# Optimization experiments

Measured on AMD Instinct MI355X. Metric: run time of the kernel, lower is better.

## Reference

```python
import jax, jax.numpy as jnp
import numpy as np

B, N, K = 8, 4096, 64          # graphs, nodes per graph, clusters
E_PER = 65536                   # edges per graph (avg degree 16)
EPS = 1e-15


def gcn_conv(x, W, b, src, dst, num_nodes):
    """PyG GCNConv: add self-loops, symmetric deg^-1/2 normalization, sum-aggregate at dst."""
    h = x @ W
    loop = jnp.arange(num_nodes, dtype=src.dtype)
    s_all = jnp.concatenate([src, loop])
    d_all = jnp.concatenate([dst, loop])
    deg = jax.ops.segment_sum(jnp.ones(d_all.shape[0], dtype=h.dtype), d_all, num_segments=num_nodes)
    dis = jnp.where(deg > 0, jax.lax.rsqrt(deg), 0.0)
    msg = h[s_all] * (dis[s_all] * dis[d_all])[:, None]
    return jax.ops.segment_sum(msg, d_all, num_segments=num_nodes) + b


def setup_inputs() -> dict:
    key = jax.random.key(0)
    ks = jax.random.split(key, 12)
    F_in, H, F_out = 128, 128, 128
    x = jax.random.normal(ks[0], (B * N, F_in), dtype=jnp.float32)
    # within-graph random edges, then offset to global node ids
    local = jax.random.randint(ks[1], (2, B * E_PER), 0, N, dtype=jnp.int32)
    offs = jnp.repeat(jnp.arange(B, dtype=jnp.int32) * N, E_PER)
    edge_index = local + offs[None, :]
    batch = jnp.repeat(jnp.arange(B, dtype=jnp.int32), N)

    def lin(k, i, o):
        return (jax.random.normal(k, (i, o), dtype=jnp.float32) / np.float32(np.sqrt(i)))

    return {
        "x": x, "edge_index": edge_index, "batch": batch,
        "W1": lin(ks[2], F_in, H), "b1": jnp.zeros((H,), jnp.float32),
        "W2": lin(ks[3], H, H),    "b2": jnp.zeros((H,), jnp.float32),
        "Wa1": lin(ks[4], H, H),   "ba1": jnp.zeros((H,), jnp.float32),
        "Wa2": lin(ks[5], H, K),   "ba2": jnp.zeros((K,), jnp.float32),
        "Wo": lin(ks[6], H, F_out), "bo": jnp.zeros((F_out,), jnp.float32),
    }


def reference(x, edge_index, batch, W1, b1, W2, b2, Wa1, ba1, Wa2, ba2, Wo, bo):
    num_nodes = B * N
    src, dst = edge_index[0], edge_index[1]
    # two GCN layers (dropout inactive in eval mode)
    h = jax.nn.relu(gcn_conv(x, W1, b1, src, dst, num_nodes))
    h = gcn_conv(h, W2, b2, src, dst, num_nodes)
    # assignment MLP + softmax (module applies softmax; dense_mincut_pool re-applies it)
    s = jax.nn.softmax(jnp.tanh(h @ Wa1 + ba1) @ Wa2 + ba2, axis=-1)
    # to_dense_adj: scatter edges into [B, N, N]
    g = src // N
    adj = jnp.zeros((B, N, N), h.dtype).at[g, src % N, dst % N].add(1.0)
    # to_dense_batch: equal-size graphs -> reshape (mask all True)
    x_d = h.reshape(B, N, -1)
    s_d = jax.nn.softmax(s.reshape(B, N, K), axis=-1)  # PyG internal softmax (double softmax, faithful)
    # dense_mincut_pool
    out = jnp.einsum('bnk,bnf->bkf', s_d, x_d)              # s^T x : [B,K,F]
    As = jnp.einsum('bnm,bmk->bnk', adj, s_d)
    out_adj = jnp.einsum('bnk,bnj->bkj', s_d, As)           # s^T A s : [B,K,K]
    mincut_num = jnp.trace(out_adj, axis1=-2, axis2=-1)
    d_flat = adj.sum(-1)                                    # node degrees
    mincut_den = jnp.einsum('bnk,bn,bnk->b', s_d, d_flat, s_d)  # trace(s^T D s)
    mincut_loss = jnp.mean(-(mincut_num / mincut_den))
    ss = jnp.einsum('bnk,bnj->bkj', s_d, s_d)
    ss_n = jnp.linalg.norm(ss, axis=(-1, -2), keepdims=True)
    i_s = jnp.eye(K, dtype=ss.dtype)
    ortho_loss = jnp.mean(jnp.linalg.norm(ss / ss_n - i_s / jnp.sqrt(jnp.float32(K)), axis=(-1, -2)))
    # zero diagonal + symmetric degree normalization of pooled adj
    out_adj = out_adj * (1.0 - i_s)
    d = jnp.sqrt(out_adj.sum(-1))[:, None, :] + EPS         # [B,1,K]
    out_adj = out_adj / d / jnp.swapaxes(d, 1, 2)
    # output projection
    pooled_x = jax.nn.relu(out.reshape(-1, out.shape[-1]) @ Wo + bo)  # [B*K, F_out]
    pooled_batch = jnp.repeat(jnp.arange(B), K)
    # pooled_adj returned densely: pooled_edge_index == nonzero(pooled_adj > 0) (dynamic shape)
    return pooled_x, out_adj, pooled_batch, mincut_loss, ortho_loss
```

## Files before the change

### kernel.cpp

```cpp
#include <hip/hip_runtime.h>

#define NNODES 32768
#define NEDGES 524288
#define KCL 64
#define CPG 16

typedef _Float16 half8v __attribute__((ext_vector_type(8)));
typedef _Float16 half4v __attribute__((ext_vector_type(4)));
typedef float floatx4 __attribute__((ext_vector_type(4)));

#define WT1_OFF   0
#define WT2_OFF   16384
#define WTA1_OFF  32768
#define WTA2_OFF  49152
#define WTO_OFF   57344
#define WT_TOTAL  73728

__device__ __forceinline__ float wave_sum(float v) {
#pragma unroll
  for (int off = 32; off > 0; off >>= 1) v += __shfl_xor(v, off, 64);
  return v;
}

__global__ __launch_bounds__(256) void hist2_kernel(const int* __restrict__ src, const int* __restrict__ dst,
                                                    int* __restrict__ pIn,
                                                    const float* __restrict__ W1, const float* __restrict__ W2,
                                                    const float* __restrict__ Wa1, const float* __restrict__ Wa2,
                                                    const float* __restrict__ Wo, _Float16* __restrict__ wt16) {
  __shared__ int hIn[4096];
  const int t = threadIdx.x;
  const int g = blockIdx.x & 7;
  const int chunk = blockIdx.x >> 3;
  const int ebase = (g << 16) + (chunk << 12);
  const int nbase = g << 12;
  for (int i = t; i < 4096; i += 256) hIn[i] = 0;
  __syncthreads();
  {
    int tg = blockIdx.x * 256 + t;
#pragma unroll
    for (int i = 0; i < 3; i++) {
      int id = tg + i * 32768;
      if (id < WT_TOTAL) {
        const float* W; int base, BN;
        if (id < 16384)      { W = W1;  base = WT1_OFF;  BN = 128; }
        else if (id < 32768) { W = W2;  base = WT2_OFF;  BN = 128; }
        else if (id < 49152) { W = Wa1; base = WTA1_OFF; BN = 128; }
        else if (id < 57344) { W = Wa2; base = WTA2_OFF; BN = 64; }
        else                 { W = Wo;  base = WTO_OFF;  BN = 128; }
        int m = id - base;
        int k = m / BN, n = m % BN;
        wt16[base + n * 128 + k] = (_Float16)W[m];
      }
    }
  }
  const int4* dst4 = reinterpret_cast<const int4*>(dst + ebase);
#pragma unroll
  for (int i = 0; i < 4; ++i) {
    int4 d = dst4[i * 256 + t];
    atomicAdd(&hIn[d.x - nbase], 1);
    atomicAdd(&hIn[d.y - nbase], 1);
    atomicAdd(&hIn[d.z - nbase], 1);
    atomicAdd(&hIn[d.w - nbase], 1);
  }
  __syncthreads();
  int* dIn = pIn + ((size_t)(g * CPG + chunk) << 12);
  for (int i = t; i < 4096; i += 256) dIn[i] = hIn[i];
}

__global__ __launch_bounds__(1024) void scan2_kernel(const int* __restrict__ pIn, int* __restrict__ offs,
                                                     int* __restrict__ cbase, float* __restrict__ dis) {
  __shared__ int part[1024];
  const int t = threadIdx.x;
  const int g = blockIdx.x;
  int tot[4];
  int s = 0;
#pragma unroll
  for (int j = 0; j < 4; ++j) {
    int l = t * 4 + j;
    int cnt = 0;
#pragma unroll
    for (int c = 0; c < CPG; ++c) cnt += pIn[(((size_t)(g * CPG + c)) << 12) + l];
    tot[j] = cnt;
    s += cnt;
  }
  part[t] = s;
  __syncthreads();
  for (int off = 1; off < 1024; off <<= 1) {
    int add = (t >= off) ? part[t - off] : 0;
    __syncthreads();
    part[t] += add;
    __syncthreads();
  }
  int run = (g << 16) + ((t == 0) ? 0 : part[t - 1]);
#pragma unroll
  for (int j = 0; j < 4; ++j) {
    int l = t * 4 + j;
    int n = (g << 12) + l;
    offs[n] = run;
    dis[n] = rsqrtf((float)tot[j] + 1.0f);
    int running = run;
#pragma unroll
    for (int c = 0; c < CPG; ++c) {
      size_t idx = (((size_t)(g * CPG + c)) << 12) + l;
      cbase[idx] = running;
      running += pIn[idx];
    }
    run += tot[j];
  }
  if (g == 0 && t == 0) offs[NNODES] = NEDGES;
}

__global__ __launch_bounds__(256) void scatter2_kernel(const int* __restrict__ src, const int* __restrict__ dst,
                                                       const int* __restrict__ cbase, int* __restrict__ ssrc) {
  __shared__ int cur[4096];
  const int t = threadIdx.x;
  const int g = blockIdx.x & 7;
  const int chunk = blockIdx.x >> 3;
  const int ebase = (g << 16) + (chunk << 12);
  const int nbase = g << 12;
  const int* cb = cbase + ((size_t)(g * CPG + chunk) << 12);
  for (int i = t; i < 4096; i += 256) cur[i] = cb[i];
  __syncthreads();
  const int4* dst4 = reinterpret_cast<const int4*>(dst + ebase);
  const int4* src4 = reinterpret_cast<const int4*>(src + ebase);
#pragma unroll
  for (int i = 0; i < 4; ++i) {
    int4 d = dst4[i * 256 + t];
    int4 s = src4[i * 256 + t];
    int p0 = atomicAdd(&cur[d.x - nbase], 1); ssrc[p0] = s.x;
    int p1 = atomicAdd(&cur[d.y - nbase], 1); ssrc[p1] = s.y;
    int p2 = atomicAdd(&cur[d.z - nbase], 1); ssrc[p2] = s.z;
    int p3 = atomicAdd(&cur[d.w - nbase], 1); ssrc[p3] = s.w;
  }
}

template <int ACT, int BIAS, int SCALE, int AFP32>
__global__ __launch_bounds__(256) void mgemm_kernel(const void* __restrict__ Ain, const _Float16* __restrict__ WT16,
                                                    const float* __restrict__ bias, const float* __restrict__ rowscale,
                                                    _Float16* __restrict__ Cout) {
  __shared__ _Float16 WT[128][136];
  const int t = threadIdx.x;
  const int lane = t & 63;
  const int quad = lane >> 4, l16 = lane & 15;
  const long rowbase = (long)(blockIdx.x & 7) * 4096 + (long)(blockIdx.x >> 3) * 128 + (t >> 6) * 32;
  half8v af[2][4];
#pragma unroll
  for (int rt = 0; rt < 2; rt++)
#pragma unroll
    for (int kt = 0; kt < 4; kt++) {
      if (AFP32) {
        const float* A32 = (const float*)Ain;
        const float* p = A32 + (rowbase + rt * 16 + l16) * 128 + kt * 32 + quad * 8;
        float4 p0 = *reinterpret_cast<const float4*>(p);
        float4 p1 = *reinterpret_cast<const float4*>(p + 4);
        half8v h = {(_Float16)p0.x, (_Float16)p0.y, (_Float16)p0.z, (_Float16)p0.w,
                    (_Float16)p1.x, (_Float16)p1.y, (_Float16)p1.z, (_Float16)p1.w};
        af[rt][kt] = h;
      } else {
        const _Float16* A16 = (const _Float16*)Ain;
        af[rt][kt] = *reinterpret_cast<const half8v*>(A16 + (rowbase + rt * 16 + l16) * 128 + kt * 32 + quad * 8);
      }
    }
#pragma unroll
  for (int i = 0; i < 8; i++) {
    int idx = i * 256 + t;
    int n = idx >> 4, k8 = (idx & 15) << 3;
    *reinterpret_cast<half8v*>(&WT[n][k8]) = *reinterpret_cast<const half8v*>(&WT16[n * 128 + k8]);
  }
  __syncthreads();
  floatx4 acc[2][8];
#pragma unroll
  for (int rt = 0; rt < 2; rt++)
#pragma unroll
    for (int ct = 0; ct < 8; ct++) acc[rt][ct] = {0.f, 0.f, 0.f, 0.f};
#pragma unroll
  for (int kt = 0; kt < 4; kt++) {
    half8v bf[8];
#pragma unroll
    for (int ct = 0; ct < 8; ct++)
      bf[ct] = *reinterpret_cast<const half8v*>(&WT[ct * 16 + l16][kt * 32 + quad * 8]);
#pragma unroll
    for (int rt = 0; rt < 2; rt++)
#pragma unroll
      for (int ct = 0; ct < 8; ct++)
        acc[rt][ct] = __builtin_amdgcn_mfma_f32_16x16x32_f16(af[rt][kt], bf[ct], acc[rt][ct], 0, 0, 0);
  }
#pragma unroll
  for (int rt = 0; rt < 2; rt++) {
#pragma unroll
    for (int r = 0; r < 4; r++) {
      long row = rowbase + rt * 16 + quad * 4 + r;
      float sc = SCALE ? rowscale[row] : 1.f;
#pragma unroll
      for (int ct = 0; ct < 8; ct++) {
        float v = acc[rt][ct][r];
        if (SCALE) v *= sc;
        if (BIAS) v += bias[ct * 16 + l16];
        if (ACT == 1) v = fmaxf(v, 0.f);
        Cout[row * 128 + ct * 16 + l16] = (_Float16)v;
      }
    }
  }
}

__global__ __launch_bounds__(256) void mlp_kernel(const _Float16* __restrict__ h2, const _Float16* __restrict__ wta1,
                                                  const _Float16* __restrict__ wta2, const float* __restrict__ ba1,
                                                  const float* __restrict__ ba2, _Float16* __restrict__ sh) {
  __shared__ _Float16 WT1[128][136];
  __shared__ _Float16 Z[64][136];
  const int t = threadIdx.x;
  const int lane = t & 63;
  const int quad = lane >> 4, l16 = lane & 15;
  const int w = t >> 6;
  const long rowbase = (long)(blockIdx.x & 7) * 4096 + (long)(blockIdx.x >> 3) * 64 + w * 16;
  half8v af[4];
#pragma unroll
  for (int kt = 0; kt < 4; kt++)
    af[kt] = *reinterpret_cast<const half8v*>(h2 + (rowbase + l16) * 128 + kt * 32 + quad * 8);
#pragma unroll
  for (int i = 0; i < 8; i++) {
    int idx = i * 256 + t;
    int n = idx >> 4, k8 = (idx & 15) << 3;
    *reinterpret_cast<half8v*>(&WT1[n][k8]) = *reinterpret_cast<const half8v*>(&wta1[n * 128 + k8]);
  }
  __syncthreads();
  {
    floatx4 acc[8];
#pragma unroll
    for (int ct = 0; ct < 8; ct++) acc[ct] = {0.f, 0.f, 0.f, 0.f};
#pragma unroll
    for (int kt = 0; kt < 4; kt++) {
#pragma unroll
      for (int ct = 0; ct < 8; ct++) {
        half8v bf = *reinterpret_cast<const half8v*>(&WT1[ct * 16 + l16][kt * 32 + quad * 8]);
        acc[ct] = __builtin_amdgcn_mfma_f32_16x16x32_f16(af[kt], bf, acc[ct], 0, 0, 0);
      }
    }
#pragma unroll
    for (int r = 0; r < 4; r++) {
      int lrow = w * 16 + quad * 4 + r;
#pragma unroll
      for (int ct = 0; ct < 8; ct++) {
        float v = tanhf(acc[ct][r] + ba1[ct * 16 + l16]);
        Z[lrow][ct * 16 + l16] = (_Float16)v;
      }
    }
  }
  __syncthreads();
#pragma unroll
  for (int i = 0; i < 4; i++) {
    int idx = i * 256 + t;
    int n = idx >> 4, k8 = (idx & 15) << 3;
    *reinterpret_cast<half8v*>(&WT1[n][k8]) = *reinterpret_cast<const half8v*>(&wta2[n * 128 + k8]);
  }
  half8v af2[4];
#pragma unroll
  for (int kt = 0; kt < 4; kt++)
    af2[kt] = *reinterpret_cast<const half8v*>(&Z[w * 16 + l16][kt * 32 + quad * 8]);
  __syncthreads();
  floatx4 acc2[4];
#pragma unroll
  for (int ct = 0; ct < 4; ct++) acc2[ct] = {0.f, 0.f, 0.f, 0.f};
#pragma unroll
  for (int kt = 0; kt < 4; kt++) {
#pragma unroll
    for (int ct = 0; ct < 4; ct++) {
      half8v bf = *reinterpret_cast<const half8v*>(&WT1[ct * 16 + l16][kt * 32 + quad * 8]);
      acc2[ct] = __builtin_amdgcn_mfma_f32_16x16x32_f16(af2[kt], bf, acc2[ct], 0, 0, 0);
    }
  }
#pragma unroll
  for (int r = 0; r < 4; r++) {
    long row = rowbase + quad * 4 + r;
    float v[4];
#pragma unroll
    for (int ct = 0; ct < 4; ct++) v[ct] = acc2[ct][r] + ba2[ct * 16 + l16];
    float m = fmaxf(fmaxf(v[0], v[1]), fmaxf(v[2], v[3]));
#pragma unroll
    for (int off = 1; off <= 8; off <<= 1) m = fmaxf(m, __shfl_xor(m, off, 64));
    float se = 0.f;
#pragma unroll
    for (int ct = 0; ct < 4; ct++) { v[ct] = __expf(v[ct] - m); se += v[ct]; }
#pragma unroll
    for (int off = 1; off <= 8; off <<= 1) se += __shfl_xor(se, off, 64);
    float inv = 1.0f / se;
#pragma unroll
    for (int ct = 0; ct < 4; ct++) v[ct] *= inv;
    float m2 = fmaxf(fmaxf(v[0], v[1]), fmaxf(v[2], v[3]));
#pragma unroll
    for (int off = 1; off <= 8; off <<= 1) m2 = fmaxf(m2, __shfl_xor(m2, off, 64));
    float se2 = 0.f;
#pragma unroll
    for (int ct = 0; ct < 4; ct++) { v[ct] = __expf(v[ct] - m2); se2 += v[ct]; }
#pragma unroll
    for (int off = 1; off <= 8; off <<= 1) se2 += __shfl_xor(se2, off, 64);
    float inv2 = 1.0f / se2;
#pragma unroll
    for (int ct = 0; ct < 4; ct++) sh[row * 64 + ct * 16 + l16] = (_Float16)(v[ct] * inv2);
  }
}

__global__ __launch_bounds__(256) void aggregate_kernel(const _Float16* __restrict__ hs, const float* __restrict__ dis,
                                                        const int* __restrict__ offs, const int* __restrict__ ssrc,
                                                        const float* __restrict__ bias, _Float16* __restrict__ outh,
                                                        int relu) {
  const int lane = threadIdx.x & 63;
  const int b = blockIdx.x;
  const int node = ((b & 7) << 12) + ((b >> 3) << 2) + (threadIdx.x >> 6);
  const int q = lane >> 4;
  const int fl = (lane & 15) * 8;
  const int e0 = offs[node], e1 = offs[node + 1];
  float fa[8];
#pragma unroll
  for (int j = 0; j < 8; j++) fa[j] = 0.f;
  int e = e0;
  for (; e + 16 <= e1; e += 16) {
    int s0 = ssrc[e + q];
    int s1 = ssrc[e + 4 + q];
    int s2 = ssrc[e + 8 + q];
    int s3 = ssrc[e + 12 + q];
    half8v v0 = *reinterpret_cast<const half8v*>(hs + (size_t)s0 * 128 + fl);
    half8v v1 = *reinterpret_cast<const half8v*>(hs + (size_t)s1 * 128 + fl);
    half8v v2 = *reinterpret_cast<const half8v*>(hs + (size_t)s2 * 128 + fl);
    half8v v3 = *reinterpret_cast<const half8v*>(hs + (size_t)s3 * 128 + fl);
#pragma unroll
    for (int j = 0; j < 8; j++) fa[j] += (float)v0[j] + (float)v1[j] + (float)v2[j] + (float)v3[j];
  }
  if (e < e1) {
    int last = e1 - 1;
    int s[4]; bool m[4];
#pragma unroll
    for (int jj = 0; jj < 4; jj++) {
      int idx = e + jj * 4 + q;
      m[jj] = idx < e1;
      int sv = ssrc[idx < last ? idx : last];
      s[jj] = m[jj] ? sv : node;
    }
#pragma unroll
    for (int jj = 0; jj < 4; jj++) {
      half8v v = *reinterpret_cast<const half8v*>(hs + (size_t)s[jj] * 128 + fl);
      if (m[jj]) {
#pragma unroll
        for (int j = 0; j < 8; j++) fa[j] += (float)v[j];
      }
    }
  }
#pragma unroll
  for (int j = 0; j < 8; j++) {
    fa[j] += __shfl_xor(fa[j], 16, 64);
    fa[j] += __shfl_xor(fa[j], 32, 64);
  }
  if (q == 0) {
    float dn = dis[node];
    half8v self = *reinterpret_cast<const half8v*>(hs + (size_t)node * 128 + fl);
    float4 b0 = *reinterpret_cast<const float4*>(bias + fl);
    float4 b1 = *reinterpret_cast<const float4*>(bias + fl + 4);
    float bb[8] = {b0.x, b0.y, b0.z, b0.w, b1.x, b1.y, b1.z, b1.w};
    half8v r;
#pragma unroll
    for (int j = 0; j < 8; j++) {
      float v = fmaf(fa[j] + (float)self[j], dn, bb[j]);
      if (relu) v = fmaxf(v, 0.f);
      r[j] = (_Float16)v;
    }
    *reinterpret_cast<half8v*>(outh + (size_t)node * 128 + fl) = r;
  }
}

__global__ __launch_bounds__(256) void gather_kernel(const _Float16* __restrict__ sh, const int* __restrict__ offs,
                                                     const int* __restrict__ ssrc, _Float16* __restrict__ Gh,
                                                     float* __restrict__ dnp) {
  const int lane = threadIdx.x & 63;
  const int b = blockIdx.x;
  const int node = ((b & 7) << 12) + ((b >> 3) << 2) + (threadIdx.x >> 6);
  const int q = lane >> 3;
  const int fl = (lane & 7) * 8;
  const int e0 = offs[node], e1 = offs[node + 1];
  float fa[8];
  float sq = 0.f;
#pragma unroll
  for (int j = 0; j < 8; j++) fa[j] = 0.f;
  int e = e0;
  for (; e + 16 <= e1; e += 16) {
    int s0 = ssrc[e + q];
    int s1 = ssrc[e + 8 + q];
    half8v v0 = *reinterpret_cast<const half8v*>(sh + (size_t)s0 * 64 + fl);
    half8v v1 = *reinterpret_cast<const half8v*>(sh + (size_t)s1 * 64 + fl);
#pragma unroll
    for (int j = 0; j < 8; j++) {
      float f0 = (float)v0[j], f1 = (float)v1[j];
      fa[j] += f0 + f1;
      sq = fmaf(f0, f0, sq);
      sq = fmaf(f1, f1, sq);
    }
  }
  if (e < e1) {
    int last = e1 - 1;
    int i0 = e + q, i1 = e + 8 + q;
    bool m0 = i0 < e1, m1 = i1 < e1;
    int sv0 = ssrc[i0 < last ? i0 : last];
    int sv1 = ssrc[i1 < last ? i1 : last];
    int s0 = m0 ? sv0 : node;
    int s1 = m1 ? sv1 : node;
    half8v v0 = *reinterpret_cast<const half8v*>(sh + (size_t)s0 * 64 + fl);
    half8v v1 = *reinterpret_cast<const half8v*>(sh + (size_t)s1 * 64 + fl);
#pragma unroll
    for (int j = 0; j < 8; j++) {
      float f0 = m0 ? (float)v0[j] : 0.f;
      float f1 = m1 ? (float)v1[j] : 0.f;
      fa[j] += f0 + f1;
      sq = fmaf(f0, f0, sq);
      sq = fmaf(f1, f1, sq);
    }
  }
#pragma unroll
  for (int j = 0; j < 8; j++) {
    fa[j] += __shfl_xor(fa[j], 8, 64);
    fa[j] += __shfl_xor(fa[j], 16, 64);
    fa[j] += __shfl_xor(fa[j], 32, 64);
  }
  float den = wave_sum(sq);
  if (lane == 0) dnp[node] = den;
  if (q == 0) {
    half8v r;
#pragma unroll
    for (int j = 0; j < 8; j++) r[j] = (_Float16)fa[j];
    *reinterpret_cast<half8v*>(Gh + (size_t)node * 64 + fl) = r;
  }
}

__global__ __launch_bounds__(512) void atb_kernel(const _Float16* __restrict__ sh, const _Float16* __restrict__ Gh,
                                                  const _Float16* __restrict__ h2, float* __restrict__ pF) {
  __shared__ _Float16 XsT[64][136];
  __shared__ _Float16 YsT[256][40];
  const int t = threadIdx.x;
  const int g = blockIdx.x & 7, chunk = blockIdx.x >> 3;
  const int n0 = g * 4096 + chunk * 128;
  const int lane = t & 63;
  const int w = t >> 6;
  const int mtile = w & 3;
  const int nhalf = w >> 2;
  const int quad = lane >> 4, l16 = lane & 15;

#pragma unroll
  for (int i = 0; i < 4; i++) {
    int slot = i * 512 + t;
    int k = slot >> 4, c4 = (slot & 15) * 4;
    half4v v = *reinterpret_cast<const half4v*>(&sh[(size_t)(n0 + k) * 64 + c4]);
#pragma unroll
    for (int j = 0; j < 4; j++) XsT[c4 + j][k] = v[j];
  }

  floatx4 acc[8];
#pragma unroll
  for (int nt = 0; nt < 8; nt++) acc[nt] = {0.f, 0.f, 0.f, 0.f};

  for (int kt = 0; kt < 4; ++kt) {
    const int nb = n0 + kt * 32;
    __syncthreads();
#pragma unroll
    for (int i = 0; i < 4; i++) {
      int slot = i * 512 + t;
      int cg = slot & 15, k = (slot >> 4) & 31, ch = slot >> 9;
      int c = ch * 64 + cg * 4;
      half4v v;
      if (c < 64)       v = *reinterpret_cast<const half4v*>(&Gh[(size_t)(nb + k) * 64 + c]);
      else if (c < 128) v = *reinterpret_cast<const half4v*>(&sh[(size_t)(nb + k) * 64 + (c - 64)]);
      else              v = *reinterpret_cast<const half4v*>(&h2[(size_t)(nb + k) * 128 + (c - 128)]);
#pragma unroll
      for (int j = 0; j < 4; j++) YsT[c + j][k] = v[j];
    }
    __syncthreads();
    half8v af = *reinterpret_cast<const half8v*>(&XsT[mtile * 16 + l16][kt * 32 + quad * 8]);
#pragma unroll
    for (int nt = 0; nt < 8; nt++) {
      half8v bf = *reinterpret_cast<const half8v*>(&YsT[(nhalf * 8 + nt) * 16 + l16][quad * 8]);
      acc[nt] = __builtin_amdgcn_mfma_f32_16x16x32_f16(af, bf, acc[nt], 0, 0, 0);
    }
  }
  float* dst = pF + (size_t)blockIdx.x * 16384;
#pragma unroll
  for (int nt = 0; nt < 8; nt++) {
#pragma unroll
    for (int r = 0; r < 4; r++) {
      dst[(mtile * 16 + quad * 4 + r) * 256 + (nhalf * 8 + nt) * 16 + l16] = acc[nt][r];
    }
  }
}

__global__ __launch_bounds__(256) void merge_kernel(const float* __restrict__ pF, float* __restrict__ oadj,
                                                    float* __restrict__ ssb, _Float16* __restrict__ outp16) {
  int g = blockIdx.x & 7;
  int o4 = (blockIdx.x >> 3) * 256 + threadIdx.x;
  float sx = 0.f, sy = 0.f, sz = 0.f, sw = 0.f;
#pragma unroll
  for (int q = 0; q < 32; ++q) {
    float4 v = *reinterpret_cast<const float4*>(pF + (size_t)(q * 8 + g) * 16384 + o4 * 4);
    sx += v.x; sy += v.y; sz += v.z; sw += v.w;
  }
  int row = o4 >> 6;
  int c = (o4 & 63) * 4;
  if (c < 64) {
    float4 o = {sx, sy, sz, sw};
    *reinterpret_cast<float4*>(&oadj[g * 4096 + row * 64 + c]) = o;
  } else if (c < 128) {
    float4 o = {sx, sy, sz, sw};
    *reinterpret_cast<float4*>(&ssb[g * 4096 + row * 64 + (c - 64)]) = o;
  } else {
    half4v h = {(_Float16)sx, (_Float16)sy, (_Float16)sz, (_Float16)sw};
    *reinterpret_cast<half4v*>(&outp16[g * 8192 + row * 128 + (c - 128)]) = h;
  }
}

__global__ __launch_bounds__(256) void epilogue2_kernel(const float* __restrict__ oadj, const float* __restrict__ ssb,
                                                        const _Float16* __restrict__ outp16, const _Float16* __restrict__ wto,
                                                        const float* __restrict__ bo, const float* __restrict__ dn,
                                                        float* __restrict__ out) {
  __shared__ _Float16 outpS[64][136];
  __shared__ _Float16 WoT[128][136];
  __shared__ float red[256];
  __shared__ float rowsum[64];
  __shared__ float dw[4], w1[4], w2[4], w3[4];
  const int g = blockIdx.x, t = threadIdx.x;

#pragma unroll
  for (int i = 0; i < 8; i++) {
    int idx = i * 256 + t;
    int n = idx >> 4, k8 = (idx & 15) << 3;
    *reinterpret_cast<half8v*>(&WoT[n][k8]) = *reinterpret_cast<const half8v*>(&wto[n * 128 + k8]);
  }
#pragma unroll
  for (int i = 0; i < 4; i++) {
    int idx = i * 256 + t;
    int orow = idx >> 4, c8 = (idx & 15) * 8;
    half8v v = *reinterpret_cast<const half8v*>(&outp16[g * 8192 + orow * 128 + c8]);
    *reinterpret_cast<half8v*>(&outpS[orow][c8]) = v;
  }

  const int row = t >> 2, p = t & 3;
  float Areg[16];
  float trs_p = 0.f, ssq_p = 0.f;
#pragma unroll
  for (int c4 = 0; c4 < 4; c4++) {
    float4 a = *reinterpret_cast<const float4*>(&oadj[g * 4096 + row * 64 + p * 16 + c4 * 4]);
    Areg[c4 * 4 + 0] = a.x; Areg[c4 * 4 + 1] = a.y; Areg[c4 * 4 + 2] = a.z; Areg[c4 * 4 + 3] = a.w;
    float4 s = *reinterpret_cast<const float4*>(&ssb[g * 4096 + row * 64 + p * 16 + c4 * 4]);
    float vv[4] = {s.x, s.y, s.z, s.w};
#pragma unroll
    for (int jj = 0; jj < 4; jj++) {
      ssq_p += vv[jj] * vv[jj];
      int col = p * 16 + c4 * 4 + jj;
      if (col == row) trs_p += vv[jj];
    }
  }
  float da = 0.f;
#pragma unroll
  for (int i = 0; i < 16; i++) da += dn[g * 4096 + i * 256 + t];
  float dws = wave_sum(da);
  if ((t & 63) == 0) dw[t >> 6] = dws;

  float rs = 0.f, tra = 0.f;
#pragma unroll
  for (int c = 0; c < 16; c++) {
    int j = p * 16 + c;
    if (j == row) tra += Areg[c];
    else rs += Areg[c];
  }
  red[t] = rs;
  __syncthreads();
  if (p == 0) rowsum[row] = red[t] + red[t + 1] + red[t + 2] + red[t + 3];
  float v1 = wave_sum(tra), v2 = wave_sum(trs_p), v3 = wave_sum(ssq_p);
  if ((t & 63) == 0) { int w = t >> 6; w1[w] = v1; w2[w] = v2; w3[w] = v3; }
  __syncthreads();
  if (t == 0) {
    float TRA = w1[0] + w1[1] + w1[2] + w1[3];
    float TRS = w2[0] + w2[1] + w2[2] + w2[3];
    float SSQ = w3[0] + w3[1] + w3[2] + w3[3];
    float DEN = dw[0] + dw[1] + dw[2] + dw[3];
    atomicAdd(&out[98816], -(TRA / DEN) * 0.125f);
    float ssn = sqrtf(SSQ);
    atomicAdd(&out[98817], sqrtf(2.0f - TRS / (4.0f * ssn)) * 0.125f);
  }
  float di = sqrtf(rowsum[row]) + 1e-15f;
#pragma unroll
  for (int c = 0; c < 16; c++) {
    int j = p * 16 + c;
    float v = (j == row) ? 0.f : Areg[c];
    float dj = sqrtf(rowsum[j]) + 1e-15f;
    out[65536 + g * 4096 + row * 64 + j] = v / (di * dj);
  }
  if (t < 64) out[98304 + g * 64 + t] = (float)g;

  const int lane = t & 63;
  const int quad = lane >> 4, l16 = lane & 15;
  const int w = t >> 6;
  floatx4 acc[8];
#pragma unroll
  for (int ct = 0; ct < 8; ct++) acc[ct] = {0.f, 0.f, 0.f, 0.f};
#pragma unroll
  for (int kt = 0; kt < 4; kt++) {
    half8v af = *reinterpret_cast<const half8v*>(&outpS[w * 16 + l16][kt * 32 + quad * 8]);
#pragma unroll
    for (int ct = 0; ct < 8; ct++) {
      half8v bf = *reinterpret_cast<const half8v*>(&WoT[ct * 16 + l16][kt * 32 + quad * 8]);
      acc[ct] = __builtin_amdgcn_mfma_f32_16x16x32_f16(af, bf, acc[ct], 0, 0, 0);
    }
  }
#pragma unroll
  for (int r = 0; r < 4; r++) {
    int orow = w * 16 + quad * 4 + r;
#pragma unroll
    for (int ct = 0; ct < 8; ct++) {
      int col = ct * 16 + l16;
      float v = fmaxf(acc[ct][r] + bo[col], 0.f);
      out[(g * 64 + orow) * 128 + col] = v;
    }
  }
}

extern "C" void kernel_launch(void* const* d_in, const int* in_sizes, int n_in,
                              void* d_out, int out_size, void* d_ws, size_t ws_size,
                              hipStream_t stream) {
  const float* x   = (const float*)d_in[0];
  const int*   ei  = (const int*)d_in[1];
  const float* W1  = (const float*)d_in[3];
  const float* b1  = (const float*)d_in[4];
  const float* W2  = (const float*)d_in[5];
  const float* b2  = (const float*)d_in[6];
  const float* Wa1 = (const float*)d_in[7];
  const float* ba1 = (const float*)d_in[8];
  const float* Wa2 = (const float*)d_in[9];
  const float* ba2 = (const float*)d_in[10];
  const float* Wo  = (const float*)d_in[11];
  const float* bo  = (const float*)d_in[12];
  const int* src = ei;
  const int* dst = ei + NEDGES;
  float* out = (float*)d_out;

  char* ws = (char*)d_ws;
  size_t o = 0;
  auto alloc = [&](size_t bytes) -> void* {
    void* p = ws + o;
    o += (bytes + 255) & ~(size_t)255;
    return p;
  };
  _Float16* h16A = (_Float16*)alloc((size_t)NNODES * 128 * 2);
  _Float16* h16B = (_Float16*)alloc((size_t)NNODES * 128 * 2);
  _Float16* h16C = (_Float16*)alloc((size_t)NNODES * 128 * 2);
  _Float16* sh   = (_Float16*)alloc((size_t)NNODES * 64 * 2);
  _Float16* Gh   = (_Float16*)alloc((size_t)NNODES * 64 * 2);
  float* pF    = (float*)alloc((size_t)256 * 16384 * 4);
  float* dis   = (float*)alloc((size_t)NNODES * 4);
  int* offs    = (int*)alloc((size_t)(NNODES + 1) * 4);
  int* ssrc    = (int*)alloc((size_t)NEDGES * 4);
  int* pIn     = (int*)alloc((size_t)8 * CPG * 4096 * 4);
  int* cbase   = (int*)alloc((size_t)8 * CPG * 4096 * 4);
  float* dn    = (float*)alloc((size_t)NNODES * 4);
  float* oadj  = (float*)alloc(8 * 4096 * 4);
  float* ssb   = (float*)alloc(8 * 4096 * 4);
  _Float16* outp16 = (_Float16*)alloc(8 * 8192 * 2);
  _Float16* wt16   = (_Float16*)alloc((size_t)WT_TOTAL * 2);

  hipMemsetAsync(out + 98816, 0, 2 * sizeof(float), stream);

  hist2_kernel<<<8 * CPG, 256, 0, stream>>>(src, dst, pIn, W1, W2, Wa1, Wa2, Wo, wt16);
  scan2_kernel<<<8, 1024, 0, stream>>>(pIn, offs, cbase, dis);
  scatter2_kernel<<<8 * CPG, 256, 0, stream>>>(src, dst, cbase, ssrc);

  mgemm_kernel<0, 0, 1, 1><<<NNODES / 128, 256, 0, stream>>>(x, wt16 + WT1_OFF, nullptr, dis, h16A);
  aggregate_kernel<<<NNODES / 4, 256, 0, stream>>>(h16A, dis, offs, ssrc, b1, h16B, 1);
  mgemm_kernel<0, 0, 1, 0><<<NNODES / 128, 256, 0, stream>>>(h16B, wt16 + WT2_OFF, nullptr, dis, h16A);
  aggregate_kernel<<<NNODES / 4, 256, 0, stream>>>(h16A, dis, offs, ssrc, b2, h16C, 0);

  mlp_kernel<<<NNODES / 64, 256, 0, stream>>>(h16C, wt16 + WTA1_OFF, wt16 + WTA2_OFF, ba1, ba2, sh);

  gather_kernel<<<NNODES / 4, 256, 0, stream>>>(sh, offs, ssrc, Gh, dn);
  atb_kernel<<<256, 512, 0, stream>>>(sh, Gh, h16C, pF);
  merge_kernel<<<128, 256, 0, stream>>>(pF, oadj, ssb, outp16);
  epilogue2_kernel<<<8, 256, 0, stream>>>(oadj, ssb, outp16, wt16 + WTO_OFF, bo, dn, out);
}
```

Before: 195.7 us.

## Fuse first GEMM into histogram kernel and apply source normalization in aggregation

The first x@W1 GEMM now runs as extra blocks of the histogram kernel. It does not depend on degrees, because the deg^-1/2 source scaling moves into the first aggregation, which reads dis[src] per edge. This removes one launch and the memset, and lets the GEMM overlap the histogram. In exchange, aggregation does an extra scattered read per edge. tanhf in the MLP is also swapped for an exp/rcp approximation.

```diff
diff --git a/kernel.cpp b/kernel.cpp
--- a/kernel.cpp
+++ b/kernel.cpp
@@ -22,49 +22,110 @@
   return v;
 }
 
-__global__ __launch_bounds__(256) void hist2_kernel(const int* __restrict__ src, const int* __restrict__ dst,
-                                                    int* __restrict__ pIn,
-                                                    const float* __restrict__ W1, const float* __restrict__ W2,
-                                                    const float* __restrict__ Wa1, const float* __restrict__ Wa2,
-                                                    const float* __restrict__ Wo, _Float16* __restrict__ wt16) {
-  __shared__ int hIn[4096];
+__global__ __launch_bounds__(256) void histgemm1_kernel(const int* __restrict__ src, const int* __restrict__ dst,
+                                                        int* __restrict__ pIn,
+                                                        const float* __restrict__ W1, const float* __restrict__ W2,
+                                                        const float* __restrict__ Wa1, const float* __restrict__ Wa2,
+                                                        const float* __restrict__ Wo, _Float16* __restrict__ wt16,
+                                                        const float* __restrict__ x, _Float16* __restrict__ h16A,
+                                                        float* __restrict__ out) {
+  __shared__ _Float16 WT[128][136];
   const int t = threadIdx.x;
-  const int g = blockIdx.x & 7;
-  const int chunk = blockIdx.x >> 3;
-  const int ebase = (g << 16) + (chunk << 12);
-  const int nbase = g << 12;
-  for (int i = t; i < 4096; i += 256) hIn[i] = 0;
-  __syncthreads();
-  {
-    int tg = blockIdx.x * 256 + t;
-#pragma unroll
-    for (int i = 0; i < 3; i++) {
-      int id = tg + i * 32768;
-      if (id < WT_TOTAL) {
-        const float* W; int base, BN;
-        if (id < 16384)      { W = W1;  base = WT1_OFF;  BN = 128; }
-        else if (id < 32768) { W = W2;  base = WT2_OFF;  BN = 128; }
-        else if (id < 49152) { W = Wa1; base = WTA1_OFF; BN = 128; }
-        else if (id < 57344) { W = Wa2; base = WTA2_OFF; BN = 64; }
-        else                 { W = Wo;  base = WTO_OFF;  BN = 128; }
-        int m = id - base;
-        int k = m / BN, n = m % BN;
-        wt16[base + n * 128 + k] = (_Float16)W[m];
-      }
-    }
-  }
-  const int4* dst4 = reinterpret_cast<const int4*>(dst + ebase);
-#pragma unroll
-  for (int i = 0; i < 4; ++i) {
-    int4 d = dst4[i * 256 + t];
-    atomicAdd(&hIn[d.x - nbase], 1);
-    atomicAdd(&hIn[d.y - nbase], 1);
-    atomicAdd(&hIn[d.z - nbase], 1);
-    atomicAdd(&hIn[d.w - nbase], 1);
-  }
-  __syncthreads();
-  int* dIn = pIn + ((size_t)(g * CPG + chunk) << 12);
-  for (int i = t; i < 4096; i += 256) dIn[i] = hIn[i];
+  if (blockIdx.x < 128) {
+    int* hIn = reinterpret_cast<int*>(&WT[0][0]);
+    const int g = blockIdx.x & 7;
+    const int chunk = blockIdx.x >> 3;
+    const int ebase = (g << 16) + (chunk << 12);
+    const int nbase = g << 12;
+    if (blockIdx.x == 0 && t < 2) out[98816 + t] = 0.f;
+    for (int i = t; i < 4096; i += 256) hIn[i] = 0;
+    __syncthreads();
+    {
+      int tg = blockIdx.x * 256 + t;
+#pragma unroll
+      for (int i = 0; i < 3; i++) {
+        int id = tg + i * 32768;
+        if (id < WT_TOTAL) {
+          const float* W; int base, BN;
+          if (id < 16384)      { W = W1;  base = WT1_OFF;  BN = 128; }
+          else if (id < 32768) { W = W2;  base = WT2_OFF;  BN = 128; }
+          else if (id < 49152) { W = Wa1; base = WTA1_OFF; BN = 128; }
+          else if (id < 57344) { W = Wa2; base = WTA2_OFF; BN = 64; }
+          else                 { W = Wo;  base = WTO_OFF;  BN = 128; }
+          int m = id - base;
+          int k = m / BN, n = m % BN;
+          wt16[base + n * 128 + k] = (_Float16)W[m];
+        }
+      }
+    }
+    const int4* dst4 = reinterpret_cast<const int4*>(dst + ebase);
+#pragma unroll
+    for (int i = 0; i < 4; ++i) {
+      int4 d = dst4[i * 256 + t];
+      atomicAdd(&hIn[d.x - nbase], 1);
+      atomicAdd(&hIn[d.y - nbase], 1);
+      atomicAdd(&hIn[d.z - nbase], 1);
+      atomicAdd(&hIn[d.w - nbase], 1);
+    }
+    __syncthreads();
+    int* dIn = pIn + ((size_t)(g * CPG + chunk) << 12);
+    for (int i = t; i < 4096; i += 256) dIn[i] = hIn[i];
+  } else {
+    const int bid = blockIdx.x - 128;
+    const int lane = t & 63;
+    const int quad = lane >> 4, l16 = lane & 15;
+    const long rowbase = (long)(bid & 7) * 4096 + (long)(bid >> 3) * 128 + (t >> 6) * 32;
+    half8v af[2][4];
+#pragma unroll
+    for (int rt = 0; rt < 2; rt++)
+#pragma unroll
+      for (int kt = 0; kt < 4; kt++) {
+        const float* p = x + (rowbase + rt * 16 + l16) * 128 + kt * 32 + quad * 8;
+        float4 p0 = *reinterpret_cast<const float4*>(p);
+        float4 p1 = *reinterpret_cast<const float4*>(p + 4);
+        half8v h = {(_Float16)p0.x, (_Float16)p0.y, (_Float16)p0.z, (_Float16)p0.w,
+                    (_Float16)p1.x, (_Float16)p1.y, (_Float16)p1.z, (_Float16)p1.w};
+        af[rt][kt] = h;
+      }
+#pragma unroll
+    for (int i = 0; i < 16; i++) {
+      int idx = i * 256 + t;
+      int k = idx >> 5, n4 = (idx & 31) << 2;
+      float4 wv = *reinterpret_cast<const float4*>(W1 + k * 128 + n4);
+      WT[n4 + 0][k] = (_Float16)wv.x;
+      WT[n4 + 1][k] = (_Float16)wv.y;
+      WT[n4 + 2][k] = (_Float16)wv.z;
+      WT[n4 + 3][k] = (_Float16)wv.w;
+    }
+    __syncthreads();
+    floatx4 acc[2][8];
+#pragma unroll
+    for (int rt = 0; rt < 2; rt++)
+#pragma unroll
+      for (int ct = 0; ct < 8; ct++) acc[rt][ct] = {0.f, 0.f, 0.f, 0.f};
+#pragma unroll
+    for (int kt = 0; kt < 4; kt++) {
+      half8v bf[8];
+#pragma unroll
+      for (int ct = 0; ct < 8; ct++)
+        bf[ct] = *reinterpret_cast<const half8v*>(&WT[ct * 16 + l16][kt * 32 + quad * 8]);
+#pragma unroll
+      for (int rt = 0; rt < 2; rt++)
+#pragma unroll
+        for (int ct = 0; ct < 8; ct++)
+          acc[rt][ct] = __builtin_amdgcn_mfma_f32_16x16x32_f16(af[rt][kt], bf[ct], acc[rt][ct], 0, 0, 0);
+    }
+#pragma unroll
+    for (int rt = 0; rt < 2; rt++) {
+#pragma unroll
+      for (int r = 0; r < 4; r++) {
+        long row = rowbase + rt * 16 + quad * 4 + r;
+#pragma unroll
+        for (int ct = 0; ct < 8; ct++)
+          h16A[row * 128 + ct * 16 + l16] = (_Float16)acc[rt][ct][r];
+      }
+    }
+  }
 }
 
 __global__ __launch_bounds__(1024) void scan2_kernel(const int* __restrict__ pIn, int* __restrict__ offs,
@@ -241,7 +302,9 @@
       int lrow = w * 16 + quad * 4 + r;
 #pragma unroll
       for (int ct = 0; ct < 8; ct++) {
-        float v = tanhf(acc[ct][r] + ba1[ct * 16 + l16]);
+        float zx = acc[ct][r] + ba1[ct * 16 + l16];
+        float ex = __expf(2.0f * zx);
+        float v = 1.0f - 2.0f * __builtin_amdgcn_rcpf(ex + 1.0f);
         Z[lrow][ct * 16 + l16] = (_Float16)v;
       }
     }
@@ -300,16 +363,17 @@
   }
 }
 
+template <int RELU, int DISSRC>
 __global__ __launch_bounds__(256) void aggregate_kernel(const _Float16* __restrict__ hs, const float* __restrict__ dis,
                                                         const int* __restrict__ offs, const int* __restrict__ ssrc,
-                                                        const float* __restrict__ bias, _Float16* __restrict__ outh,
-                                                        int relu) {
+                                                        const float* __restrict__ bias, _Float16* __restrict__ outh) {
   const int lane = threadIdx.x & 63;
   const int b = blockIdx.x;
   const int node = ((b & 7) << 12) + ((b >> 3) << 2) + (threadIdx.x >> 6);
   const int q = lane >> 4;
   const int fl = (lane & 15) * 8;
   const int e0 = offs[node], e1 = offs[node + 1];
+  const float dn = dis[node];
   float fa[8];
 #pragma unroll
   for (int j = 0; j < 8; j++) fa[j] = 0.f;
@@ -319,12 +383,23 @@
     int s1 = ssrc[e + 4 + q];
     int s2 = ssrc[e + 8 + q];
     int s3 = ssrc[e + 12 + q];
+    float d0 = 1.f, d1 = 1.f, d2 = 1.f, d3 = 1.f;
+    if (DISSRC) { d0 = dis[s0]; d1 = dis[s1]; d2 = dis[s2]; d3 = dis[s3]; }
     half8v v0 = *reinterpret_cast<const half8v*>(hs + (size_t)s0 * 128 + fl);
     half8v v1 = *reinterpret_cast<const half8v*>(hs + (size_t)s1 * 128 + fl);
     half8v v2 = *reinterpret_cast<const half8v*>(hs + (size_t)s2 * 128 + fl);
     half8v v3 = *reinterpret_cast<const half8v*>(hs + (size_t)s3 * 128 + fl);
 #pragma unroll
-    for (int j = 0; j < 8; j++) fa[j] += (float)v0[j] + (float)v1[j] + (float)v2[j] + (float)v3[j];
+    for (int j = 0; j < 8; j++) {
+      if (DISSRC) {
+        fa[j] = fmaf(d0, (float)v0[j], fa[j]);
+        fa[j] = fmaf(d1, (float)v1[j], fa[j]);
+        fa[j] = fmaf(d2, (float)v2[j], fa[j]);
+        fa[j] = fmaf(d3, (float)v3[j], fa[j]);
+      } else {
+        fa[j] += (float)v0[j] + (float)v1[j] + (float)v2[j] + (float)v3[j];
+      }
+    }
   }
   if (e < e1) {
     int last = e1 - 1;
@@ -339,9 +414,13 @@
 #pragma unroll
     for (int jj = 0; jj < 4; jj++) {
       half8v v = *reinterpret_cast<const half8v*>(hs + (size_t)s[jj] * 128 + fl);
+      float ds = DISSRC ? dis[s[jj]] : 1.f;
       if (m[jj]) {
 #pragma unroll
-        for (int j = 0; j < 8; j++) fa[j] += (float)v[j];
+        for (int j = 0; j < 8; j++) {
+          if (DISSRC) fa[j] = fmaf(ds, (float)v[j], fa[j]);
+          else fa[j] += (float)v[j];
+        }
       }
     }
   }
@@ -351,7 +430,6 @@
     fa[j] += __shfl_xor(fa[j], 32, 64);
   }
   if (q == 0) {
-    float dn = dis[node];
     half8v self = *reinterpret_cast<const half8v*>(hs + (size_t)node * 128 + fl);
     float4 b0 = *reinterpret_cast<const float4*>(bias + fl);
     float4 b1 = *reinterpret_cast<const float4*>(bias + fl + 4);
@@ -359,8 +437,11 @@
     half8v r;
 #pragma unroll
     for (int j = 0; j < 8; j++) {
-      float v = fmaf(fa[j] + (float)self[j], dn, bb[j]);
-      if (relu) v = fmaxf(v, 0.f);
+      float acc = fa[j];
+      if (DISSRC) acc = fmaf(dn, (float)self[j], acc);
+      else acc += (float)self[j];
+      float v = fmaf(acc, dn, bb[j]);
+      if (RELU) v = fmaxf(v, 0.f);
       r[j] = (_Float16)v;
     }
     *reinterpret_cast<half8v*>(outh + (size_t)node * 128 + fl) = r;
@@ -661,16 +742,13 @@
   _Float16* outp16 = (_Float16*)alloc(8 * 8192 * 2);
   _Float16* wt16   = (_Float16*)alloc((size_t)WT_TOTAL * 2);
 
-  hipMemsetAsync(out + 98816, 0, 2 * sizeof(float), stream);
-
-  hist2_kernel<<<8 * CPG, 256, 0, stream>>>(src, dst, pIn, W1, W2, Wa1, Wa2, Wo, wt16);
+  histgemm1_kernel<<<384, 256, 0, stream>>>(src, dst, pIn, W1, W2, Wa1, Wa2, Wo, wt16, x, h16A, out);
   scan2_kernel<<<8, 1024, 0, stream>>>(pIn, offs, cbase, dis);
   scatter2_kernel<<<8 * CPG, 256, 0, stream>>>(src, dst, cbase, ssrc);
 
-  mgemm_kernel<0, 0, 1, 1><<<NNODES / 128, 256, 0, stream>>>(x, wt16 + WT1_OFF, nullptr, dis, h16A);
-  aggregate_kernel<<<NNODES / 4, 256, 0, stream>>>(h16A, dis, offs, ssrc, b1, h16B, 1);
+  aggregate_kernel<1, 1><<<NNODES / 4, 256, 0, stream>>>(h16A, dis, offs, ssrc, b1, h16B);
   mgemm_kernel<0, 0, 1, 0><<<NNODES / 128, 256, 0, stream>>>(h16B, wt16 + WT2_OFF, nullptr, dis, h16A);
-  aggregate_kernel<<<NNODES / 4, 256, 0, stream>>>(h16A, dis, offs, ssrc, b2, h16C, 0);
+  aggregate_kernel<0, 0><<<NNODES / 4, 256, 0, stream>>>(h16A, dis, offs, ssrc, b2, h16C);
 
   mlp_kernel<<<NNODES / 64, 256, 0, stream>>>(h16C, wt16 + WTA1_OFF, wt16 + WTA2_OFF, ba1, ba2, sh);
 
```

Result: no change. 194.0 us (-0.9%).
